# Kernel tuning notes

Hardware: AMD Instinct MI355X
Metric: run time of the kernel (lower is better)

Reference implementation:

```python
import jax, jax.numpy as jnp
import numpy as np

D = 256; NH = 8; NL = 4; NP = 8; DFF = 1024; NQ = 300; BS = 8
DH = D // NH
_SHAPES = np.array([[100, 100], [50, 50], [25, 25], [13, 13]], dtype=np.int64)
S = int(_SHAPES.prod(1).sum())


def setup_inputs():
    key = jax.random.key(0)
    ks = jax.random.split(key, 24)
    rn = lambda k, sh, s=0.02: jax.random.normal(k, sh, jnp.float32) * s
    lsi = np.concatenate([[0], np.cumsum(_SHAPES.prod(1))[:-1]])
    return {
        'tgt': rn(ks[0], (NQ, BS, D), 1.0),
        'tgt_query_mask': rn(ks[1], (NQ, BS, D), 1.0),
        'tgt_reference_bboxs': jax.random.uniform(ks[2], (NQ, BS, 4), jnp.float32, 0.1, 0.5),
        'tgt_reference_masks': jax.random.uniform(ks[3], (NQ, BS, 32, 32), jnp.float32),
        'memory': rn(ks[4], (S, BS, D), 1.0),
        'in_proj_w': rn(ks[5], (3 * D, D)), 'in_proj_b': jnp.zeros((3 * D,), jnp.float32),
        'out_sa_w': rn(ks[6], (D, D)), 'out_sa_b': jnp.zeros((D,), jnp.float32),
        'norm2_g': jnp.ones((D,), jnp.float32), 'norm2_b': jnp.zeros((D,), jnp.float32),
        'value_w': rn(ks[7], (D, D)), 'value_b': jnp.zeros((D,), jnp.float32),
        'off_w': rn(ks[8], (NH * NL * NP * 2, D)), 'off_b': rn(ks[9], (NH * NL * NP * 2,), 0.5),
        'aw_w': rn(ks[10], (NH * NL * NP, D)), 'aw_b': jnp.zeros((NH * NL * NP,), jnp.float32),
        'out_ca_w': rn(ks[11], (D, D)), 'out_ca_b': jnp.zeros((D,), jnp.float32),
        'norm1_g': jnp.ones((D,), jnp.float32), 'norm1_b': jnp.zeros((D,), jnp.float32),
        'lin1_w': rn(ks[12], (DFF, D)), 'lin1_b': jnp.zeros((DFF,), jnp.float32),
        'lin2_w': rn(ks[13], (D, DFF)), 'lin2_b': jnp.zeros((D,), jnp.float32),
        'norm3_g': jnp.ones((D,), jnp.float32), 'norm3_b': jnp.zeros((D,), jnp.float32),
        'memory_key_padding_mask': jnp.zeros((BS, S), bool),
        'memory_spatial_shapes': jnp.asarray(_SHAPES, jnp.int32),
        'memory_level_start_index': jnp.asarray(lsi, jnp.int32),
    }


def _lin(x, w, b):
    return x @ w.T + b


def _ln(x, g, b):
    mu = x.mean(-1, keepdims=True)
    v = ((x - mu) ** 2).mean(-1, keepdims=True)
    return (x - mu) / jnp.sqrt(v + 1e-5) * g + b


def _ms_deform(query, ref, mem, pad_mask, spatial, lstart, vw, vb, ow, ob, aww, awb, outw, outb):
    # query/ref/mem: (bs, nq, D), (bs, nq, 4 cxcywh in [0,1]), (bs, S, D)
    bs, nq, _ = query.shape
    value = _lin(mem, vw, vb)
    value = jnp.where(pad_mask[:, :, None], 0.0, value).reshape(bs, -1, NH, DH)
    off = _lin(query, ow, ob).reshape(bs, nq, NH, NL, NP, 2)
    aw = jax.nn.softmax(_lin(query, aww, awb).reshape(bs, nq, NH, NL * NP), -1)
    aw = aw.reshape(bs, nq, NH, NL, NP)
    ref6 = ref[:, :, None, None, None, :]
    loc = ref6[..., :2] + off / NP * ref6[..., 2:4] * 0.5  # (bs,nq,NH,NL,NP,2)
    Hs = spatial[:, 0].reshape(1, 1, 1, NL, 1)
    Ws = spatial[:, 1].reshape(1, 1, 1, NL, 1)
    ls = lstart.reshape(1, 1, 1, NL, 1)
    Hf = Hs.astype(jnp.float32); Wf = Ws.astype(jnp.float32)
    # grid_sample align_corners=False pixel coords
    x = loc[..., 0] * Wf - 0.5
    y = loc[..., 1] * Hf - 0.5
    x0 = jnp.floor(x); y0 = jnp.floor(y)
    vT = value.transpose(2, 0, 1, 3)  # (NH,bs,S,DH)
    acc = jnp.zeros((bs, nq, NH, NL, NP, DH), jnp.float32)
    for dx in (0.0, 1.0):
        for dy in (0.0, 1.0):
            xi = x0 + dx; yi = y0 + dy
            w = (1.0 - jnp.abs(x - xi)) * (1.0 - jnp.abs(y - yi))
            valid = ((xi >= 0) & (xi < Wf) & (yi >= 0) & (yi < Hf)).astype(jnp.float32)
            xc = jnp.clip(xi, 0.0, Wf - 1.0).astype(jnp.int32)
            yc = jnp.clip(yi, 0.0, Hf - 1.0).astype(jnp.int32)
            idx = ls + yc * Ws + xc  # flat index into S, (bs,nq,NH,NL,NP)
            iT = idx.transpose(2, 0, 1, 3, 4).reshape(NH, bs, -1)
            g = jax.vmap(lambda v, i: jnp.take_along_axis(v, i[:, :, None], axis=1))(vT, iT)
            g = g.reshape(NH, bs, nq, NL, NP, DH).transpose(1, 2, 0, 3, 4, 5)
            acc = acc + (w * valid)[..., None] * g
    out = (acc * aw[..., None]).sum(axis=(3, 4)).reshape(bs, nq, D)
    return _lin(out, outw, outb)


def reference(tgt, tgt_query_mask, tgt_reference_bboxs, tgt_reference_masks, memory,
              in_proj_w, in_proj_b, out_sa_w, out_sa_b, norm2_g, norm2_b,
              value_w, value_b, off_w, off_b, aw_w, aw_b, out_ca_w, out_ca_b,
              norm1_g, norm1_b, lin1_w, lin1_b, lin2_w, lin2_b, norm3_g, norm3_b,
              memory_key_padding_mask, memory_spatial_shapes, memory_level_start_index):
    nq, bs, _ = tgt.shape
    # --- self attention (nn.MultiheadAttention, seq-first, eval mode) ---
    q = tgt + tgt_query_mask
    qh = _lin(q, in_proj_w[:D], in_proj_b[:D]).reshape(nq, bs, NH, DH)
    kh = _lin(q, in_proj_w[D:2 * D], in_proj_b[D:2 * D]).reshape(nq, bs, NH, DH)
    vh = _lin(tgt, in_proj_w[2 * D:], in_proj_b[2 * D:]).reshape(nq, bs, NH, DH)
    logits = jnp.einsum('qbhd,kbhd->bhqk', qh, kh) / np.sqrt(DH).astype(np.float32)
    attn = jax.nn.softmax(logits, -1)
    sa = jnp.einsum('bhqk,kbhd->qbhd', attn, vh).reshape(nq, bs, D)
    sa = _lin(sa, out_sa_w, out_sa_b)
    tgt = _ln(tgt + sa, norm2_g, norm2_b)
    # --- multi-scale deformable cross attention ---
    ca = _ms_deform((tgt + tgt_query_mask).transpose(1, 0, 2),
                    tgt_reference_bboxs.transpose(1, 0, 2),
                    memory.transpose(1, 0, 2),
                    memory_key_padding_mask, memory_spatial_shapes, memory_level_start_index,
                    value_w, value_b, off_w, off_b, aw_w, aw_b, out_ca_w, out_ca_b)
    tgt = _ln(tgt + ca.transpose(1, 0, 2), norm1_g, norm1_b)
    # --- FFN ---
    t2 = _lin(jax.nn.relu(_lin(tgt, lin1_w, lin1_b)), lin2_w, lin2_b)
    return _ln(tgt + t2, norm3_g, norm3_b)
```

## Files before the change

### kernel.cpp

```cpp
#include <hip/hip_runtime.h>
#include <hip/hip_bf16.h>
#include <math.h>

#define NQ 300
#define BSZ 8
#define DIM 256
#define NHEAD 8
#define ROWS 2400

typedef __attribute__((ext_vector_type(8))) short bf16x8;
typedef __attribute__((ext_vector_type(4))) float f32x4;

__device__ inline short f2bf(float f) {
  __hip_bfloat16 h = __float2bfloat16(f);
  return *reinterpret_cast<short*>(&h);
}
__device__ inline float bf2f(unsigned short u) {
  union { unsigned u; float f; } c;
  c.u = ((unsigned)u) << 16;
  return c.f;
}

#if __has_builtin(__builtin_amdgcn_global_load_lds)
__device__ inline void gld16(const void* gsrc, void* ldst, int lane) {
  (void)lane;
  auto g = (const __attribute__((address_space(1))) unsigned int*)gsrc;
  auto l = (__attribute__((address_space(3))) unsigned int*)ldst;
  __builtin_amdgcn_global_load_lds(g, l, 16, 0, 0);
}
#else
__device__ inline void gld16(const void* gsrc, void* ldst, int lane) {
  ((float4*)ldst)[lane] = *(const float4*)gsrc;
}
#endif

__device__ inline bf16x8 cvt8(float4 v0, float4 v1) {
  bf16x8 o;
  o[0] = f2bf(v0.x); o[1] = f2bf(v0.y); o[2] = f2bf(v0.z); o[3] = f2bf(v0.w);
  o[4] = f2bf(v1.x); o[5] = f2bf(v1.y); o[6] = f2bf(v1.z); o[7] = f2bf(v1.w);
  return o;
}

struct WEntry { const float* src; unsigned short* dst; int K; int gstart; };
struct WPack { WEntry e[8]; int total; };
__global__ __launch_bounds__(256) void wconv_kernel(WPack P) {
  int g = blockIdx.x * 256 + threadIdx.x;
  if (g >= P.total) return;
  int i = 0;
  while (i < 7 && g >= P.e[i + 1].gstart) ++i;
  const float* src = P.e[i].src;
  unsigned short* dst = P.e[i].dst;
  const int K = P.e[i].K;
  int gl = g - P.e[i].gstart;
  int gpr = K >> 3;
  int r = gl / gpr, gk = gl - r * gpr;
  int nb = r >> 6, rr = r & 63;
  int c = gk >> 3, g8 = gk & 7;
  const float* s = src + (size_t)r * K + gk * 8;
  float4 v0 = *(const float4*)s, v1 = *(const float4*)(s + 4);
  size_t byte = ((size_t)(nb * (K >> 6) + c) * 64 + rr) * 128 + ((g8 * 16) ^ ((rr & 7) << 4));
  *(bf16x8*)((char*)dst + byte) = cvt8(v0, v1);
}

__global__ void bias_cat(const float* __restrict__ a, const float* __restrict__ b,
                         float* __restrict__ o) {
  int t = blockIdx.x * 256 + threadIdx.x;
  if (t < 512) o[t] = a[t];
  else if (t < 768) o[t] = b[t - 512];
}

template <bool VMASK>
__global__ __launch_bounds__(256) void vgemm(const float* __restrict__ A,
                                             const unsigned short* __restrict__ Wz,
                                             const float* __restrict__ bias,
                                             __hip_bfloat16* __restrict__ C, int M,
                                             const unsigned char* __restrict__ vmask,
                                             int Srows) {
  __shared__ char As[2][16384];
  __shared__ char Bsh[2][16384];
  const int tid = threadIdx.x, lane = tid & 63, wid = tid >> 6;
  const int wr = wid >> 1, wc = wid & 1;
  const int nb = blockIdx.x;
  const int m0 = blockIdx.y * 128;
  const int l15 = lane & 15, lk = lane >> 4;

  f32x4 acc[4][4];
#pragma unroll
  for (int i = 0; i < 4; ++i)
#pragma unroll
    for (int j = 0; j < 4; ++j) acc[i][j] = {0.f, 0.f, 0.f, 0.f};

  const float* asrc[4];
  int awby[4];
#pragma unroll
  for (int j = 0; j < 4; ++j) {
    int gb = j * 256 + tid;
    int row = gb >> 3, g8 = gb & 7;
    int rg = m0 + row;
    if (rg > M - 1) rg = M - 1;
    asrc[j] = A + (size_t)rg * 256 + g8 * 8;
    awby[j] = row * 128 + ((g8 * 16) ^ ((row & 7) << 4));
  }

  float4 ar[8];
#define V_AISSUE(c)                                        \
  {                                                        \
    _Pragma("unroll") for (int j = 0; j < 4; ++j) {        \
      const float* p = asrc[j] + (c) * 64;                 \
      ar[2 * j] = *(const float4*)p;                       \
      ar[2 * j + 1] = *(const float4*)(p + 4);             \
    }                                                      \
  }
#define V_AWRITE(buf)                                      \
  {                                                        \
    _Pragma("unroll") for (int j = 0; j < 4; ++j)          \
        *(bf16x8*)((buf) + awby[j]) = cvt8(ar[2 * j], ar[2 * j + 1]); \
  }
#define V_BGLD(c, buf)                                                          \
  {                                                                             \
    _Pragma("unroll") for (int i = 0; i < 4; ++i) {                             \
      int bch = wid * 4 + i;                                                    \
      const char* src = (const char*)Wz +                                       \
                        ((size_t)((2 * nb + (bch >> 3)) * 4 + (c))) * 8192 +    \
                        (bch & 7) * 1024 + lane * 16;                           \
      gld16(src, (buf) + bch * 1024, lane);                                     \
    }                                                                           \
  }
#define V_COMPUTE(Ab, Bb)                                                        \
  {                                                                              \
    _Pragma("unroll") for (int kk = 0; kk < 2; ++kk) {                           \
      bf16x8 af[4], bfr[4];                                                      \
      _Pragma("unroll") for (int i = 0; i < 4; ++i) {                            \
        int rr = wr * 64 + i * 16 + l15;                                         \
        af[i] = *(bf16x8*)((Ab) + rr * 128 + (((kk * 4 + lk) * 16) ^ ((rr & 7) << 4))); \
      }                                                                          \
      _Pragma("unroll") for (int j = 0; j < 4; ++j) {                            \
        int rr = wc * 64 + j * 16 + l15;                                         \
        bfr[j] = *(bf16x8*)((Bb) + (rr >> 6) * 8192 + (rr & 63) * 128 +          \
                            (((kk * 4 + lk) * 16) ^ ((rr & 7) << 4)));           \
      }                                                                          \
      _Pragma("unroll") for (int i = 0; i < 4; ++i)                              \
          _Pragma("unroll") for (int j = 0; j < 4; ++j)                          \
              acc[i][j] = __builtin_amdgcn_mfma_f32_16x16x32_bf16(af[i], bfr[j], \
                                                                  acc[i][j], 0, 0, 0); \
    }                                                                            \
  }

  V_AISSUE(0);
  V_BGLD(0, Bsh[0]);
  V_AWRITE(As[0]);
  __syncthreads();
#pragma unroll
  for (int c = 0; c < 4; ++c) {
    const int cur = c & 1;
    if (c < 3) {
      V_AISSUE(c + 1);
      V_BGLD(c + 1, Bsh[cur ^ 1]);
    }
    V_COMPUTE(As[cur], Bsh[cur]);
    if (c < 3) {
      V_AWRITE(As[cur ^ 1]);
      __syncthreads();
    }
  }

#pragma unroll
  for (int i = 0; i < 4; ++i) {
#pragma unroll
    for (int r = 0; r < 4; ++r) {
      int row = m0 + wr * 64 + i * 16 + lk * 4 + r;
      if (row >= M) continue;
      float mfac = 1.f;
      if (VMASK) mfac = vmask[(size_t)(row & 7) * Srows + (row >> 3)] ? 0.f : 1.f;
#pragma unroll
      for (int j = 0; j < 4; ++j) {
        int col = nb * 128 + wc * 64 + j * 16 + l15;
        float v = acc[i][j][r] + bias[col];
        if (VMASK) v *= mfac;
        C[(size_t)row * 256 + col] = __float2bfloat16(v);
      }
    }
  }
}

template <int BM, bool RELU, bool ADDM, bool QKV>
__global__ __launch_bounds__(256) void sgemm(const float* __restrict__ A,
                                             const float* __restrict__ Am,
                                             const unsigned short* __restrict__ Wz,
                                             const float* __restrict__ bias,
                                             float* __restrict__ C0, float* __restrict__ C1,
                                             int M, int Ns, int K) {
  constexpr int WMT = BM / 2, AM = WMT / 16, NA = BM / 32;
  __shared__ char As[2][BM * 128];
  __shared__ char Bsh[2][8192];
  const int tid = threadIdx.x, lane = tid & 63, wid = tid >> 6;
  const int wr = wid >> 1, wc = wid & 1;
  const int nb = blockIdx.x, m0 = blockIdx.y * BM;
  const int l15 = lane & 15, lk = lane >> 4;
  const bool useM = QKV ? (nb < 8) : ADDM;

  f32x4 acc[AM][2];
#pragma unroll
  for (int i = 0; i < AM; ++i)
#pragma unroll
    for (int j = 0; j < 2; ++j) acc[i][j] = {0.f, 0.f, 0.f, 0.f};

  const int nch = K >> 6;
  const float* asrc[NA];
  const float* amsrc[NA];
  int awby[NA];
  bool avalid[NA];
#pragma unroll
  for (int j = 0; j < NA; ++j) {
    int gb = j * 256 + tid;
    int row = gb >> 3, g8 = gb & 7;
    int rg = m0 + row;
    avalid[j] = rg < M;
    if (rg > M - 1) rg = M - 1;
    asrc[j] = A + (size_t)rg * K + g8 * 8;
    amsrc[j] = (useM ? Am : A) + (size_t)rg * K + g8 * 8;
    awby[j] = row * 128 + ((g8 * 16) ^ ((row & 7) << 4));
  }

  float4 ar[2 * NA], am2[2 * NA];
#define S_AISSUE(c)                                          \
  {                                                          \
    _Pragma("unroll") for (int j = 0; j < NA; ++j) {         \
      const float* p = asrc[j] + (c) * 64;                   \
      ar[2 * j] = *(const float4*)p;                         \
      ar[2 * j + 1] = *(const float4*)(p + 4);               \
      if (useM) {                                            \
        const float* q = amsrc[j] + (c) * 64;                \
        am2[2 * j] = *(const float4*)q;                      \
        am2[2 * j + 1] = *(const float4*)(q + 4);            \
      }                                                      \
    }                                                        \
  }
#define S_AWRITE(buf)                                                       \
  {                                                                         \
    _Pragma("unroll") for (int j = 0; j < NA; ++j) {                        \
      float4 v0 = ar[2 * j], v1 = ar[2 * j + 1];                            \
      if (useM) {                                                           \
        float4 w0 = am2[2 * j], w1 = am2[2 * j + 1];                        \
        v0.x += w0.x; v0.y += w0.y; v0.z += w0.z; v0.w += w0.w;             \
        v1.x += w1.x; v1.y += w1.y; v1.z += w1.z; v1.w += w1.w;             \
      }                                                                     \
      if (!avalid[j]) { v0 = make_float4(0.f,0.f,0.f,0.f); v1 = v0; }       \
      *(bf16x8*)((buf) + awby[j]) = cvt8(v0, v1);                           \
    }                                                                       \
  }
#define S_BGLD(c, buf)                                                        \
  {                                                                           \
    _Pragma("unroll") for (int i = 0; i < 2; ++i) {                           \
      int bch = wid * 2 + i;                                                  \
      const char* src = (const char*)Wz + ((size_t)(nb * nch + (c))) * 8192 + \
                        bch * 1024 + lane * 16;                               \
      gld16(src, (buf) + bch * 1024, lane);                                   \
    }                                                                         \
  }
#define S_COMPUTE(Ab, Bb)                                                        \
  {                                                                              \
    _Pragma("unroll") for (int kk = 0; kk < 2; ++kk) {                           \
      bf16x8 af[AM], bfr[2];                                                     \
      _Pragma("unroll") for (int i = 0; i < AM; ++i) {                           \
        int rr = wr * WMT + i * 16 + l15;                                        \
        af[i] = *(bf16x8*)((Ab) + rr * 128 + (((kk * 4 + lk) * 16) ^ ((rr & 7) << 4))); \
      }                                                                          \
      _Pragma("unroll") for (int j = 0; j < 2; ++j) {                            \
        int rr = wc * 32 + j * 16 + l15;                                         \
        bfr[j] = *(bf16x8*)((Bb) + rr * 128 + (((kk * 4 + lk) * 16) ^ ((rr & 7) << 4))); \
      }                                                                          \
      _Pragma("unroll") for (int i = 0; i < AM; ++i)                             \
          _Pragma("unroll") for (int j = 0; j < 2; ++j)                          \
              acc[i][j] = __builtin_amdgcn_mfma_f32_16x16x32_bf16(af[i], bfr[j], \
                                                                  acc[i][j], 0, 0, 0); \
    }                                                                            \
  }

  S_AISSUE(0);
  S_BGLD(0, Bsh[0]);
  S_AWRITE(As[0]);
  __syncthreads();
  for (int c = 0; c < nch; ++c) {
    const int cur = c & 1;
    if (c < nch - 1) {
      S_AISSUE(c + 1);
      S_BGLD(c + 1, Bsh[cur ^ 1]);
    }
    S_COMPUTE(As[cur], Bsh[cur]);
    if (c < nch - 1) {
      S_AWRITE(As[cur ^ 1]);
      __syncthreads();
    }
  }

  float* outp;
  int ostride, ocol0;
  if (QKV) {
    if (nb < 8) { outp = C0; ostride = 512; ocol0 = nb * 64; }
    else        { outp = C1; ostride = 256; ocol0 = (nb - 8) * 64; }
  } else {
    outp = C0; ostride = Ns; ocol0 = nb * 64;
  }
#pragma unroll
  for (int i = 0; i < AM; ++i) {
#pragma unroll
    for (int r = 0; r < 4; ++r) {
      int row = m0 + wr * WMT + i * 16 + lk * 4 + r;
      if (row >= M) continue;
#pragma unroll
      for (int j = 0; j < 2; ++j) {
        int cl = wc * 32 + j * 16 + l15;
        float v = acc[i][j][r] + bias[nb * 64 + cl];
        if (RELU) v = fmaxf(v, 0.f);
        outp[(size_t)row * ostride + ocol0 + cl] = v;
      }
    }
  }
}

__global__ __launch_bounds__(256) void attn_kernel(const float* __restrict__ cqk,
                                                   const float* __restrict__ cv,
                                                   float* __restrict__ out) {
  __shared__ float Ks[NQ][32];
  __shared__ float Vs[NQ][32];
  const int b = blockIdx.x, h = blockIdx.y, qt = blockIdx.z;
  const int tid = threadIdx.x;
  for (int i = tid; i < NQ * 8; i += 256) {
    int qi = i >> 3, c4 = (i & 7) * 4;
    *(float4*)&Ks[qi][c4] = *(const float4*)&cqk[((size_t)(qi * 8 + b)) * 512 + 256 + h * 32 + c4];
    *(float4*)&Vs[qi][c4] = *(const float4*)&cv[((size_t)(qi * 8 + b)) * 256 + h * 32 + c4];
  }
  __syncthreads();
  const int row = qt * 64 + (tid >> 2);
  const int qr = tid & 3;
  if (row >= NQ) return;
  float qv[8];
  const float* qptr = &cqk[((size_t)(row * 8 + b)) * 512 + h * 32 + qr * 8];
  *(float4*)&qv[0] = *(const float4*)&qptr[0];
  *(float4*)&qv[4] = *(const float4*)&qptr[4];
  const float scale = 0.17677669529663687f;
  float m = -3.0e38f, l = 0.f;
  float acc[8] = {0.f, 0.f, 0.f, 0.f, 0.f, 0.f, 0.f, 0.f};
  for (int k = 0; k < NQ; ++k) {
    const float* kr = &Ks[k][qr * 8];
    float p = 0.f;
#pragma unroll
    for (int j = 0; j < 8; ++j) p = fmaf(qv[j], kr[j], p);
    p += __shfl_xor(p, 1, 4);
    p += __shfl_xor(p, 2, 4);
    float s = p * scale;
    float mn = fmaxf(m, s);
    float corr = __expf(m - mn);
    float e = __expf(s - mn);
    l = l * corr + e;
    const float* vr = &Vs[k][qr * 8];
#pragma unroll
    for (int j = 0; j < 8; ++j) acc[j] = fmaf(acc[j], corr, e * vr[j]);
    m = mn;
  }
  float inv = 1.f / l;
  float* op = &out[((size_t)(row * 8 + b)) * 256 + h * 32 + qr * 8];
#pragma unroll
  for (int j = 0; j < 8; ++j) op[j] = acc[j] * inv;
}

__global__ __launch_bounds__(256) void resid_ln_kernel(const float* __restrict__ X,
                                                       const float* __restrict__ R,
                                                       const float* __restrict__ g,
                                                       const float* __restrict__ be,
                                                       float* __restrict__ out) {
  const int r = blockIdx.x, c = threadIdx.x;
  const size_t i = (size_t)r * 256 + c;
  float x = X[i] + R[i];
  float s = x;
#pragma unroll
  for (int o = 32; o; o >>= 1) s += __shfl_xor(s, o, 64);
  __shared__ float sm[4], sv[4];
  const int w = c >> 6;
  if ((c & 63) == 0) sm[w] = s;
  __syncthreads();
  float mu = (sm[0] + sm[1] + sm[2] + sm[3]) * (1.f / 256.f);
  float d = x - mu;
  float v = d * d;
#pragma unroll
  for (int o = 32; o; o >>= 1) v += __shfl_xor(v, o, 64);
  if ((c & 63) == 0) sv[w] = v;
  __syncthreads();
  float var = (sv[0] + sv[1] + sv[2] + sv[3]) * (1.f / 256.f);
  out[i] = d * (1.f / sqrtf(var + 1e-5f)) * g[c] + be[c];
}

__global__ __launch_bounds__(256) void deform_kernel(const unsigned short* __restrict__ value,
                                                     const float* __restrict__ offaw,
                                                     const float* __restrict__ bbox,
                                                     const int* __restrict__ spatial,
                                                     const int* __restrict__ lstart,
                                                     float* __restrict__ out, int S) {
  __shared__ int sH[4], sW[4], sL[4];
  __shared__ float sbb[4];
  const int r = blockIdx.x;
  const int b = r & 7;
  const int tid = threadIdx.x;
  if (tid < 4) {
    sH[tid] = spatial[tid * 2];
    sW[tid] = spatial[tid * 2 + 1];
    sL[tid] = lstart[tid];
    sbb[tid] = bbox[(size_t)r * 4 + tid];
  }
  __syncthreads();
  const float cx = sbb[0], cy = sbb[1], bw = sbb[2], bh = sbb[3];
  float ox = offaw[(size_t)r * 768 + (size_t)tid * 2];
  float oy = offaw[(size_t)r * 768 + (size_t)tid * 2 + 1];
  float a = offaw[(size_t)r * 768 + 512 + tid];
  float mx = a;
#pragma unroll
  for (int o = 16; o; o >>= 1) mx = fmaxf(mx, __shfl_xor(mx, o, 32));
  float e = __expf(a - mx);
  float ssum = e;
#pragma unroll
  for (int o = 16; o; o >>= 1) ssum += __shfl_xor(ssum, o, 32);
  float myaw = e / ssum;

  float acc = 0.f;
  const size_t vb = (size_t)b * 256 + (size_t)tid;
  for (int lp = 0; lp < 32; ++lp) {
    const int l = lp >> 3;
    float bx = __shfl(ox, lp, 32);
    float by = __shfl(oy, lp, 32);
    float alp = __shfl(myaw, lp, 32);
    const float Wf = (float)sW[l], Hf = (float)sH[l];
    const int ls = sL[l], Wi = sW[l];
    float lx = cx + bx * 0.0625f * bw;
    float ly = cy + by * 0.0625f * bh;
    float x = lx * Wf - 0.5f;
    float y = ly * Hf - 0.5f;
    float x0 = floorf(x), y0 = floorf(y);
    float fx = x - x0, fy = y - y0;
    float tap = 0.f;
#pragma unroll
    for (int t = 0; t < 4; ++t) {
      float xi = x0 + (float)(t & 1);
      float yi = y0 + (float)(t >> 1);
      if (xi >= 0.f && yi >= 0.f && xi < Wf && yi < Hf) {
        float wx = (t & 1) ? fx : (1.f - fx);
        float wy = (t >> 1) ? fy : (1.f - fy);
        int idx = ls + (int)yi * Wi + (int)xi;
        tap = fmaf(wx * wy, bf2f(value[(size_t)idx * 2048 + vb]), tap);
      }
    }
    acc = fmaf(alp, tap, acc);
  }
  out[(size_t)r * 256 + tid] = acc;
}

extern "C" void kernel_launch(void* const* d_in, const int* in_sizes, int n_in, void* d_out,
                              int out_size, void* d_ws, size_t ws_size, hipStream_t stream) {
  (void)n_in; (void)out_size; (void)ws_size;
  const float* tgt = (const float*)d_in[0];
  const float* qmask = (const float*)d_in[1];
  const float* bbox = (const float*)d_in[2];
  const float* memory = (const float*)d_in[4];
  const float* ipw = (const float*)d_in[5];
  const float* ipb = (const float*)d_in[6];
  const float* osw = (const float*)d_in[7];
  const float* osb = (const float*)d_in[8];
  const float* n2g = (const float*)d_in[9];
  const float* n2b = (const float*)d_in[10];
  const float* vw = (const float*)d_in[11];
  const float* vbi = (const float*)d_in[12];
  const float* ow = (const float*)d_in[13];
  const float* ob = (const float*)d_in[14];
  const float* aww = (const float*)d_in[15];
  const float* awb = (const float*)d_in[16];
  const float* ocw = (const float*)d_in[17];
  const float* ocb = (const float*)d_in[18];
  const float* n1g = (const float*)d_in[19];
  const float* n1b = (const float*)d_in[20];
  const float* l1w = (const float*)d_in[21];
  const float* l1b = (const float*)d_in[22];
  const float* l2w = (const float*)d_in[23];
  const float* l2b = (const float*)d_in[24];
  const float* n3g = (const float*)d_in[25];
  const float* n3b = (const float*)d_in[26];
  const unsigned char* kpmask = (const unsigned char*)d_in[27];
  const int* spatial = (const int*)d_in[28];
  const int* lstart = (const int*)d_in[29];
  float* out = (float*)d_out;

  const int S = in_sizes[4] / (BSZ * DIM);
  const int Mv = S * BSZ;

  float* ws = (float*)d_ws;
  size_t o = 0;
  unsigned short* value = (unsigned short*)(ws + o); o += (size_t)Mv * DIM / 2;
  float* cqk = ws + o; o += (size_t)ROWS * 512;
  float* cv = ws + o; o += (size_t)ROWS * DIM;
  float* sraw = ws + o; o += (size_t)ROWS * DIM;
  float* proj = ws + o; o += (size_t)ROWS * DIM;
  float* tgt2 = ws + o; o += (size_t)ROWS * DIM;
  float* tgt3 = ws + o; o += (size_t)ROWS * DIM;
  float* ffn1 = ws + o; o += (size_t)ROWS * 1024;
  float* offaw = ws + o; o += (size_t)ROWS * 768;
  float* obaw = ws + o; o += 768;
  unsigned short* wz = (unsigned short*)(ws + o);
  unsigned short* ipw_z = wz;
  unsigned short* osw_z = ipw_z + 768 * 256;
  unsigned short* vw_z  = osw_z + 256 * 256;
  unsigned short* ow_z  = vw_z + 256 * 256;
  unsigned short* aww_z = ow_z + 512 * 256;
  unsigned short* ocw_z = aww_z + 256 * 256;
  unsigned short* l1w_z = ocw_z + 256 * 256;
  unsigned short* l2w_z = l1w_z + 1024 * 256;

  WPack P;
  int gs = 0;
  auto ent = [&](int idx, const float* s, unsigned short* d, int N_, int K_) {
    P.e[idx] = {s, d, K_, gs};
    gs += N_ * K_ / 8;
  };
  ent(0, ipw, ipw_z, 768, 256);
  ent(1, osw, osw_z, 256, 256);
  ent(2, vw, vw_z, 256, 256);
  ent(3, ow, ow_z, 512, 256);
  ent(4, aww, aww_z, 256, 256);
  ent(5, ocw, ocw_z, 256, 256);
  ent(6, l1w, l1w_z, 1024, 256);
  ent(7, l2w, l2w_z, 256, 1024);
  P.total = gs;
  wconv_kernel<<<dim3((gs + 255) / 256), 256, 0, stream>>>(P);
  bias_cat<<<dim3(3), 256, 0, stream>>>(ob, awb, obaw);

  sgemm<64, false, false, true><<<dim3(12, 38), 256, 0, stream>>>(
      tgt, qmask, ipw_z, ipb, cqk, cv, ROWS, 0, 256);
  attn_kernel<<<dim3(BSZ, NHEAD, (NQ + 63) / 64), 256, 0, stream>>>(cqk, cv, sraw);
  sgemm<32, false, false, false><<<dim3(4, 75), 256, 0, stream>>>(
      sraw, nullptr, osw_z, osb, proj, nullptr, ROWS, 256, 256);
  resid_ln_kernel<<<ROWS, 256, 0, stream>>>(proj, tgt, n2g, n2b, tgt2);
  vgemm<true><<<dim3(2, (Mv + 127) / 128), 256, 0, stream>>>(
      memory, vw_z, vbi, (__hip_bfloat16*)value, Mv, kpmask, S);
  sgemm<64, false, true, false><<<dim3(12, 38), 256, 0, stream>>>(
      tgt2, qmask, ow_z, obaw, offaw, nullptr, ROWS, 768, 256);
  deform_kernel<<<ROWS, 256, 0, stream>>>(value, offaw, bbox, spatial, lstart, sraw, S);
  sgemm<32, false, false, false><<<dim3(4, 75), 256, 0, stream>>>(
      sraw, nullptr, ocw_z, ocb, proj, nullptr, ROWS, 256, 256);
  resid_ln_kernel<<<ROWS, 256, 0, stream>>>(proj, tgt2, n1g, n1b, tgt3);
  sgemm<64, true, false, false><<<dim3(16, 38), 256, 0, stream>>>(
      tgt3, nullptr, l1w_z, l1b, ffn1, nullptr, ROWS, 1024, 256);
  sgemm<32, false, false, false><<<dim3(4, 75), 256, 0, stream>>>(
      ffn1, nullptr, l2w_z, l2b, proj, nullptr, ROWS, 256, 1024);
  resid_ln_kernel<<<ROWS, 256, 0, stream>>>(proj, tgt3, n3g, n3b, out);
}
```

Before: 429.2 us.

## Load GEMM weight fragments directly from global memory instead of LDS staging

The weight conversion kernel now writes plain row-major bf16 instead of a swizzled tile layout. Both GEMM kernels drop the LDS double-buffer for B and have each lane read its bf16x8 weight fragments straight from global memory, relying on cache since the weights are small. The value GEMM also moves to 512 threads with 8 waves, each computing a 64x32 sub-tile. This cuts LDS traffic and async-copy overhead, but exposes global-load latency inside the MFMA loop and issues redundant weight reads across waves.

```diff
diff --git a/kernel.cpp b/kernel.cpp
--- a/kernel.cpp
+++ b/kernel.cpp
@@ -20,20 +20,6 @@
   c.u = ((unsigned)u) << 16;
   return c.f;
 }
-
-#if __has_builtin(__builtin_amdgcn_global_load_lds)
-__device__ inline void gld16(const void* gsrc, void* ldst, int lane) {
-  (void)lane;
-  auto g = (const __attribute__((address_space(1))) unsigned int*)gsrc;
-  auto l = (__attribute__((address_space(3))) unsigned int*)ldst;
-  __builtin_amdgcn_global_load_lds(g, l, 16, 0, 0);
-}
-#else
-__device__ inline void gld16(const void* gsrc, void* ldst, int lane) {
-  ((float4*)ldst)[lane] = *(const float4*)gsrc;
-}
-#endif
-
 __device__ inline bf16x8 cvt8(float4 v0, float4 v1) {
   bf16x8 o;
   o[0] = f2bf(v0.x); o[1] = f2bf(v0.y); o[2] = f2bf(v0.z); o[3] = f2bf(v0.w);
@@ -48,18 +34,10 @@
   if (g >= P.total) return;
   int i = 0;
   while (i < 7 && g >= P.e[i + 1].gstart) ++i;
-  const float* src = P.e[i].src;
-  unsigned short* dst = P.e[i].dst;
-  const int K = P.e[i].K;
   int gl = g - P.e[i].gstart;
-  int gpr = K >> 3;
-  int r = gl / gpr, gk = gl - r * gpr;
-  int nb = r >> 6, rr = r & 63;
-  int c = gk >> 3, g8 = gk & 7;
-  const float* s = src + (size_t)r * K + gk * 8;
+  const float* s = P.e[i].src + (size_t)gl * 8;
   float4 v0 = *(const float4*)s, v1 = *(const float4*)(s + 4);
-  size_t byte = ((size_t)(nb * (K >> 6) + c) * 64 + rr) * 128 + ((g8 * 16) ^ ((rr & 7) << 4));
-  *(bf16x8*)((char*)dst + byte) = cvt8(v0, v1);
+  ((bf16x8*)P.e[i].dst)[gl] = cvt8(v0, v1);
 }
 
 __global__ void bias_cat(const float* __restrict__ a, const float* __restrict__ b,
@@ -70,94 +48,82 @@
 }
 
 template <bool VMASK>
-__global__ __launch_bounds__(256) void vgemm(const float* __restrict__ A,
-                                             const unsigned short* __restrict__ Wz,
+__global__ __launch_bounds__(512) void vgemm(const float* __restrict__ A,
+                                             const unsigned short* __restrict__ Wb,
                                              const float* __restrict__ bias,
                                              __hip_bfloat16* __restrict__ C, int M,
                                              const unsigned char* __restrict__ vmask,
                                              int Srows) {
   __shared__ char As[2][16384];
-  __shared__ char Bsh[2][16384];
   const int tid = threadIdx.x, lane = tid & 63, wid = tid >> 6;
-  const int wr = wid >> 1, wc = wid & 1;
+  const int wr = wid >> 2, wc = wid & 3;
   const int nb = blockIdx.x;
   const int m0 = blockIdx.y * 128;
   const int l15 = lane & 15, lk = lane >> 4;
 
-  f32x4 acc[4][4];
+  f32x4 acc[4][2];
 #pragma unroll
   for (int i = 0; i < 4; ++i)
 #pragma unroll
-    for (int j = 0; j < 4; ++j) acc[i][j] = {0.f, 0.f, 0.f, 0.f};
-
-  const float* asrc[4];
-  int awby[4];
-#pragma unroll
-  for (int j = 0; j < 4; ++j) {
-    int gb = j * 256 + tid;
+    for (int j = 0; j < 2; ++j) acc[i][j] = {0.f, 0.f, 0.f, 0.f};
+
+  const float* asrc[2];
+  int awby[2];
+#pragma unroll
+  for (int j = 0; j < 2; ++j) {
+    int gb = j * 512 + tid;
     int row = gb >> 3, g8 = gb & 7;
     int rg = m0 + row;
     if (rg > M - 1) rg = M - 1;
     asrc[j] = A + (size_t)rg * 256 + g8 * 8;
     awby[j] = row * 128 + ((g8 * 16) ^ ((row & 7) << 4));
   }
-
-  float4 ar[8];
-#define V_AISSUE(c)                                        \
-  {                                                        \
-    _Pragma("unroll") for (int j = 0; j < 4; ++j) {        \
-      const float* p = asrc[j] + (c) * 64;                 \
-      ar[2 * j] = *(const float4*)p;                       \
-      ar[2 * j + 1] = *(const float4*)(p + 4);             \
-    }                                                      \
-  }
-#define V_AWRITE(buf)                                      \
-  {                                                        \
-    _Pragma("unroll") for (int j = 0; j < 4; ++j)          \
-        *(bf16x8*)((buf) + awby[j]) = cvt8(ar[2 * j], ar[2 * j + 1]); \
-  }
-#define V_BGLD(c, buf)                                                          \
-  {                                                                             \
-    _Pragma("unroll") for (int i = 0; i < 4; ++i) {                             \
-      int bch = wid * 4 + i;                                                    \
-      const char* src = (const char*)Wz +                                       \
-                        ((size_t)((2 * nb + (bch >> 3)) * 4 + (c))) * 8192 +    \
-                        (bch & 7) * 1024 + lane * 16;                           \
-      gld16(src, (buf) + bch * 1024, lane);                                     \
-    }                                                                           \
-  }
-#define V_COMPUTE(Ab, Bb)                                                        \
+  const char* bsrc[2];
+#pragma unroll
+  for (int j = 0; j < 2; ++j) {
+    int rr = nb * 128 + wc * 32 + j * 16 + l15;
+    bsrc[j] = (const char*)Wb + (size_t)rr * 512 + lk * 16;
+  }
+
+  float4 ar[4];
+#define V_AISSUE(c)                                 \
+  {                                                 \
+    _Pragma("unroll") for (int j = 0; j < 2; ++j) { \
+      const float* p = asrc[j] + (c) * 64;          \
+      ar[2 * j] = *(const float4*)p;                \
+      ar[2 * j + 1] = *(const float4*)(p + 4);      \
+    }                                               \
+  }
+#define V_AWRITE(buf)                                                  \
+  {                                                                    \
+    _Pragma("unroll") for (int j = 0; j < 2; ++j)                      \
+        *(bf16x8*)((buf) + awby[j]) = cvt8(ar[2 * j], ar[2 * j + 1]);  \
+  }
+#define V_COMPUTE(Ab, c)                                                         \
   {                                                                              \
     _Pragma("unroll") for (int kk = 0; kk < 2; ++kk) {                           \
-      bf16x8 af[4], bfr[4];                                                      \
+      bf16x8 af[4], bfr[2];                                                      \
+      _Pragma("unroll") for (int j = 0; j < 2; ++j)                              \
+          bfr[j] = *(const bf16x8*)(bsrc[j] + (c) * 128 + kk * 64);              \
       _Pragma("unroll") for (int i = 0; i < 4; ++i) {                            \
         int rr = wr * 64 + i * 16 + l15;                                         \
         af[i] = *(bf16x8*)((Ab) + rr * 128 + (((kk * 4 + lk) * 16) ^ ((rr & 7) << 4))); \
       }                                                                          \
-      _Pragma("unroll") for (int j = 0; j < 4; ++j) {                            \
-        int rr = wc * 64 + j * 16 + l15;                                         \
-        bfr[j] = *(bf16x8*)((Bb) + (rr >> 6) * 8192 + (rr & 63) * 128 +          \
-                            (((kk * 4 + lk) * 16) ^ ((rr & 7) << 4)));           \
-      }                                                                          \
       _Pragma("unroll") for (int i = 0; i < 4; ++i)                              \
-          _Pragma("unroll") for (int j = 0; j < 4; ++j)                          \
+          _Pragma("unroll") for (int j = 0; j < 2; ++j)                          \
               acc[i][j] = __builtin_amdgcn_mfma_f32_16x16x32_bf16(af[i], bfr[j], \
                                                                   acc[i][j], 0, 0, 0); \
     }                                                                            \
   }
 
   V_AISSUE(0);
-  V_BGLD(0, Bsh[0]);
   V_AWRITE(As[0]);
   __syncthreads();
 #pragma unroll
   for (int c = 0; c < 4; ++c) {
     const int cur = c & 1;
-    if (c < 3) {
-      V_AISSUE(c + 1);
-      V_BGLD(c + 1, Bsh[cur ^ 1]);
-    }
-    V_COMPUTE(As[cur], Bsh[cur]);
+    if (c < 3) V_AISSUE(c + 1);
+    V_COMPUTE(As[cur], c);
     if (c < 3) {
       V_AWRITE(As[cur ^ 1]);
       __syncthreads();
@@ -173,8 +139,8 @@
       float mfac = 1.f;
       if (VMASK) mfac = vmask[(size_t)(row & 7) * Srows + (row >> 3)] ? 0.f : 1.f;
 #pragma unroll
-      for (int j = 0; j < 4; ++j) {
-        int col = nb * 128 + wc * 64 + j * 16 + l15;
+      for (int j = 0; j < 2; ++j) {
+        int col = nb * 128 + wc * 32 + j * 16 + l15;
         float v = acc[i][j][r] + bias[col];
         if (VMASK) v *= mfac;
         C[(size_t)row * 256 + col] = __float2bfloat16(v);
@@ -186,13 +152,12 @@
 template <int BM, bool RELU, bool ADDM, bool QKV>
 __global__ __launch_bounds__(256) void sgemm(const float* __restrict__ A,
                                              const float* __restrict__ Am,
-                                             const unsigned short* __restrict__ Wz,
+                                             const unsigned short* __restrict__ Wb,
                                              const float* __restrict__ bias,
                                              float* __restrict__ C0, float* __restrict__ C1,
                                              int M, int Ns, int K) {
   constexpr int WMT = BM / 2, AM = WMT / 16, NA = BM / 32;
   __shared__ char As[2][BM * 128];
-  __shared__ char Bsh[2][8192];
   const int tid = threadIdx.x, lane = tid & 63, wid = tid >> 6;
   const int wr = wid >> 1, wc = wid & 1;
   const int nb = blockIdx.x, m0 = blockIdx.y * BM;
@@ -220,6 +185,12 @@
     asrc[j] = A + (size_t)rg * K + g8 * 8;
     amsrc[j] = (useM ? Am : A) + (size_t)rg * K + g8 * 8;
     awby[j] = row * 128 + ((g8 * 16) ^ ((row & 7) << 4));
+  }
+  const char* bsrc[2];
+#pragma unroll
+  for (int j = 0; j < 2; ++j) {
+    int rr = nb * 64 + wc * 32 + j * 16 + l15;
+    bsrc[j] = (const char*)Wb + (size_t)rr * (K * 2) + lk * 16;
   }
 
   float4 ar[2 * NA], am2[2 * NA];
@@ -249,26 +220,15 @@
       *(bf16x8*)((buf) + awby[j]) = cvt8(v0, v1);                           \
     }                                                                       \
   }
-#define S_BGLD(c, buf)                                                        \
-  {                                                                           \
-    _Pragma("unroll") for (int i = 0; i < 2; ++i) {                           \
-      int bch = wid * 2 + i;                                                  \
-      const char* src = (const char*)Wz + ((size_t)(nb * nch + (c))) * 8192 + \
-                        bch * 1024 + lane * 16;                               \
-      gld16(src, (buf) + bch * 1024, lane);                                   \
-    }                                                                         \
-  }
-#define S_COMPUTE(Ab, Bb)                                                        \
+#define S_COMPUTE(Ab, c)                                                         \
   {                                                                              \
     _Pragma("unroll") for (int kk = 0; kk < 2; ++kk) {                           \
       bf16x8 af[AM], bfr[2];                                                     \
+      _Pragma("unroll") for (int j = 0; j < 2; ++j)                              \
+          bfr[j] = *(const bf16x8*)(bsrc[j] + (c) * 128 + kk * 64);              \
       _Pragma("unroll") for (int i = 0; i < AM; ++i) {                           \
         int rr = wr * WMT + i * 16 + l15;                                        \
         af[i] = *(bf16x8*)((Ab) + rr * 128 + (((kk * 4 + lk) * 16) ^ ((rr & 7) << 4))); \
-      }                                                                          \
-      _Pragma("unroll") for (int j = 0; j < 2; ++j) {                            \
-        int rr = wc * 32 + j * 16 + l15;                                         \
-        bfr[j] = *(bf16x8*)((Bb) + rr * 128 + (((kk * 4 + lk) * 16) ^ ((rr & 7) << 4))); \
       }                                                                          \
       _Pragma("unroll") for (int i = 0; i < AM; ++i)                             \
           _Pragma("unroll") for (int j = 0; j < 2; ++j)                          \
@@ -278,16 +238,12 @@
   }
 
   S_AISSUE(0);
-  S_BGLD(0, Bsh[0]);
   S_AWRITE(As[0]);
   __syncthreads();
   for (int c = 0; c < nch; ++c) {
     const int cur = c & 1;
-    if (c < nch - 1) {
-      S_AISSUE(c + 1);
-      S_BGLD(c + 1, Bsh[cur ^ 1]);
-    }
-    S_COMPUTE(As[cur], Bsh[cur]);
+    if (c < nch - 1) S_AISSUE(c + 1);
+    S_COMPUTE(As[cur], c);
     if (c < nch - 1) {
       S_AWRITE(As[cur ^ 1]);
       __syncthreads();
@@ -537,7 +493,7 @@
   sgemm<32, false, false, false><<<dim3(4, 75), 256, 0, stream>>>(
       sraw, nullptr, osw_z, osb, proj, nullptr, ROWS, 256, 256);
   resid_ln_kernel<<<ROWS, 256, 0, stream>>>(proj, tgt, n2g, n2b, tgt2);
-  vgemm<true><<<dim3(2, (Mv + 127) / 128), 256, 0, stream>>>(
+  vgemm<true><<<dim3(2, (Mv + 127) / 128), 512, 0, stream>>>(
       memory, vw_z, vbi, (__hip_bfloat16*)value, Mv, kpmask, S);
   sgemm<64, false, true, false><<<dim3(12, 38), 256, 0, stream>>>(
       tgt2, qmask, ow_z, obaw, offaw, nullptr, ROWS, 768, 256);
```

Measured after the change: 455.9 us. +6.2%, slower.
